# Performance work log

Measured on AMD Instinct MI355X. Metric: run time of the kernel, lower is better.

The kernel has to match this reference:

```python
import jax, jax.numpy as jnp
import numpy as np

DEPTH = 16
PERCENT = 1.2
MAX_P = 5.0
# ps[t] = clip((t+1)*percent, 0, max_percent), as in the torch __init__
PS = np.clip((np.arange(DEPTH) + 1) * PERCENT, 0.0, MAX_P)


def setup_inputs() -> dict:
    key = jax.random.key(0)
    kx, kA = jax.random.split(key, 2)
    B, M, N = 16384, 256, 1024
    A = jax.random.normal(kA, (M, N), dtype=jnp.float32) / np.sqrt(M)
    # L = max eigenvalue of A^T A (as max_eig in the torch code), scaled by 1.001
    gram = np.asarray(A.T @ A)
    L = float(np.linalg.eigvalsh(gram)[-1]) * 1.001
    # init=True initialization: every bias layer weight is A.T / L, threshold = 1/L
    W = jnp.tile((A.T / L)[None, :, :], (DEPTH, 1, 1))  # [depth, N, M]
    threshold = jnp.ones((DEPTH,), dtype=jnp.float32) / L
    x = jax.random.normal(kx, (B, M), dtype=jnp.float32)
    return {"x": x, "A": A, "W": W, "threshold": threshold}


def _shrink(x, t):
    # soft threshold: sign(x) * max(|x| - t, 0)
    return jnp.sign(x) * jnp.maximum(jnp.abs(x) - t, 0.0)


def _shrinkss(x, t, p):
    # support-selection shrink: entries above both the learned threshold and the
    # per-row (100-p) percentile of |x| pass through untouched; the rest are
    # soft-thresholded. Mask and percentile are detached (no_grad in torch).
    n = x.shape[1]
    idx = int(np.ceil((100.0 - p) / 100.0 * n)) - 1  # static per iteration
    abs_x = jnp.abs(x)
    thresh = jax.lax.stop_gradient(jnp.sort(abs_x, axis=1)[:, idx])  # [B]
    mask = jax.lax.stop_gradient(
        ((abs_x >= t) & (abs_x >= thresh[:, None])).astype(x.dtype)
    )
    return mask * x + _shrink((1.0 - mask) * x, t)


def reference(x, A, W, threshold):
    # x: [B, M], A: [M, N], W: [depth, N, M], threshold: [depth]
    B = x.shape[0]
    N = A.shape[1]
    u = jnp.zeros((B, N), dtype=x.dtype)
    for i in range(DEPTH):
        r = x - u @ A.T                      # residual in measurement space [B, M]
        v = u + r @ W[i].T                   # gradient step via learned bias [B, N]
        u = _shrinkss(v, threshold[i], PS[i])
    return u
```

## Files before the change

### kernel.cpp

```cpp
#include <hip/hip_runtime.h>
#include <hip/hip_bf16.h>

#define B_ROWS 16384
#define M_DIM  256
#define N_DIM  1024
#define DEPTH  16

typedef __attribute__((ext_vector_type(8))) short short8;
typedef __attribute__((ext_vector_type(4))) float f32x4;
typedef __attribute__((ext_vector_type(2))) float f32x2;

#define ATP_OFF_B   0
#define WTP_OFF_B   1572864
#define RP_OFF_B    (1572864 + 25165824)
#define TAU_OFF_B   (RP_OFF_B + 25165824)
#define WS_FAST_NEED ((size_t)TAU_OFF_B + 65536)
#define WTP_SLICE   (64 * 8 * 3 * 512)
#define RP_PANEL_US 24576

#define AT_OFF 0
#define WT_OFF (262144)
#define WS_OLD_NEED ((size_t)(262144 + 16 * 262144) * 4)

__device__ __forceinline__ unsigned short bf16r(float f) {
    unsigned u = __float_as_uint(f);
    u += 0x7fffu + ((u >> 16) & 1u);
    return (unsigned short)(u >> 16);
}
__device__ __forceinline__ float bf2f(unsigned short h) {
    return __uint_as_float(((unsigned)h) << 16);
}
__device__ __forceinline__ void split3(float x, unsigned short& h, unsigned short& m,
                                       unsigned short& lo) {
    h = bf16r(x); float r1 = x - bf2f(h);
    m = bf16r(r1); float r2 = r1 - bf2f(m);
    lo = bf16r(r2);
}
__device__ __forceinline__ f32x4 MF(short8 a, short8 b, f32x4 c) {
    return __builtin_amdgcn_mfma_f32_16x16x32_bf16(a, b, c, 0, 0, 0);
}
__device__ __forceinline__ float shrink_one(float v, float t, float thrv) {
    float a = fabsf(v);
    return (a >= thrv) ? v : copysignf(fmaxf(a - t, 0.0f), v);
}

__global__ void prep_a_kernel(const float* __restrict__ A, unsigned short* __restrict__ ATp) {
    int g = blockIdx.x * 256 + threadIdx.x;
    if (g >= 16 * 32 * 64) return;
    int l = g & 63, kc = (g >> 6) & 31, tile = g >> 11;
    int row = tile * 16 + (l & 15);
    int k0 = kc * 32 + ((l >> 4) << 3);
    unsigned short h[8], m[8], lo[8];
#pragma unroll
    for (int j = 0; j < 8; ++j) split3(A[(size_t)row * N_DIM + k0 + j], h[j], m[j], lo[j]);
    size_t base = ((size_t)(tile * 32 + kc) * 3) * 512 + l * 8;
#pragma unroll
    for (int j = 0; j < 8; ++j) {
        ATp[base + j] = h[j];
        ATp[base + 512 + j] = m[j];
        ATp[base + 1024 + j] = lo[j];
    }
}

__global__ void prep_w_kernel(const float* __restrict__ W, unsigned short* __restrict__ WTp) {
    int g = blockIdx.x * 256 + threadIdx.x;
    if (g >= 16 * 64 * 8 * 64) return;
    int l = g & 63, kc = (g >> 6) & 7, tile = (g >> 9) & 63, it = g >> 15;
    int n = tile * 16 + (l & 15);
    int m0 = kc * 32 + ((l >> 4) << 3);
    const float* Wi = W + (size_t)it * N_DIM * M_DIM;
    unsigned short h[8], m[8], lo[8];
#pragma unroll
    for (int j = 0; j < 8; ++j) split3(Wi[(size_t)n * M_DIM + m0 + j], h[j], m[j], lo[j]);
    size_t base = (((size_t)(it * 64 + tile) * 8 + kc) * 3) * 512 + l * 8;
#pragma unroll
    for (int j = 0; j < 8; ++j) {
        WTp[base + j] = h[j];
        WTp[base + 512 + j] = m[j];
        WTp[base + 1024 + j] = lo[j];
    }
}

__global__ void prep_x_kernel(const float* __restrict__ x, unsigned short* __restrict__ RP) {
    int g = blockIdx.x * 256 + threadIdx.x;
    if (g >= 524288) return;
    int l = g & 63, kcp = (g >> 6) & 3, wm = (g >> 8) & 1, c = (g >> 9) & 1, panel = g >> 10;
    int row = panel * 32 + wm * 16 + (l & 15);
    int k0 = c * 128 + kcp * 32 + ((l >> 4) << 3);
    unsigned short h[8], m[8], lo[8];
#pragma unroll
    for (int j = 0; j < 8; ++j) split3(x[(size_t)row * M_DIM + k0 + j], h[j], m[j], lo[j]);
    size_t base = (size_t)panel * RP_PANEL_US + ((((c * 2 + wm) * 4 + kcp) * 3)) * 512 + l * 8;
#pragma unroll
    for (int j = 0; j < 8; ++j) {
        RP[base + j] = h[j];
        RP[base + 512 + j] = m[j];
        RP[base + 1024 + j] = lo[j];
    }
}

#define LSTR2 136
#define BUFUS 13056

__global__ __launch_bounds__(1024)
void g1_kernel(const float* __restrict__ UV, const float* __restrict__ x,
               const unsigned short* __restrict__ ATp,
               const float* __restrict__ thr_all, float* __restrict__ TAU,
               unsigned short* __restrict__ RP, int iter, int kth_prev) {
    __align__(16) __shared__ unsigned short smem[2 * BUFUS];
    __shared__ float tau_s[32];
    const int tid = threadIdx.x;
    const int l = tid & 63, w = tid >> 6;
    const int wm = w >> 3, wn = w & 7;
    const int panel = blockIdx.x;
    const int row0 = panel * 32;
    const int arow = 16 * wm + (l & 15);
    const int akl  = (l >> 4) << 3;
    const float tprev = thr_all[iter - 1];

    {
#pragma unroll 1
        for (int rr = 0; rr < 2; ++rr) {
            const int row = w * 2 + rr;
            const float* vp = UV + (size_t)(row0 + row) * N_DIM;
            unsigned key[16];
#pragma unroll
            for (int j = 0; j < 16; ++j)
                key[j] = __float_as_uint(vp[l + 64 * j]) & 0x7fffffffu;
            unsigned p = 0;
#pragma unroll 1
            for (int b = 30; b >= 0; --b) {
                const unsigned cand = p | (1u << b);
                int cnt = 0;
#pragma unroll
                for (int j = 0; j < 16; ++j) cnt += (key[j] >= cand) ? 1 : 0;
#pragma unroll
                for (int off = 32; off; off >>= 1) cnt += __shfl_xor(cnt, off);
                if (cnt >= kth_prev) p = cand;
            }
            if (l == 0) {
                tau_s[row] = __uint_as_float(p);
                TAU[row0 + row] = __uint_as_float(p);
            }
        }
    }
    __syncthreads();

    f32x4 acc_hi[2], acc_rest[2];
    double acc64[2][4];
#pragma unroll
    for (int t = 0; t < 2; ++t) {
        acc_hi[t] = (f32x4){0, 0, 0, 0};
        acc_rest[t] = (f32x4){0, 0, 0, 0};
#pragma unroll
        for (int e = 0; e < 4; ++e) acc64[t][e] = 0.0;
    }

    f32x2 st[2];
#pragma unroll
    for (int jj = 0; jj < 2; ++jj) {
        const int idx = tid + 1024 * jj;
        const int r = idx >> 6, kq = idx & 63;
        st[jj] = *(const f32x2*)&UV[(size_t)(row0 + r) * N_DIM + kq * 2];
    }
#pragma unroll
    for (int jj = 0; jj < 2; ++jj) {
        const int idx = tid + 1024 * jj;
        const int r = idx >> 6, kq = idx & 63;
        const float thrv = fmaxf(tprev, tau_s[r]);
        const float a0 = shrink_one(st[jj].x, tprev, thrv);
        const float a1 = shrink_one(st[jj].y, tprev, thrv);
        unsigned short h0, m0, lo0, h1, m1, lo1;
        split3(a0, h0, m0, lo0);
        split3(a1, h1, m1, lo1);
        const unsigned off = (unsigned)r * LSTR2 + kq * 2;
        *(unsigned*)&smem[off] = (unsigned)h0 | ((unsigned)h1 << 16);
        *(unsigned*)&smem[4352 + off] = (unsigned)m0 | ((unsigned)m1 << 16);
        *(unsigned*)&smem[8704 + off] = (unsigned)lo0 | ((unsigned)lo1 << 16);
    }
#pragma unroll
    for (int jj = 0; jj < 2; ++jj) {
        const int idx = tid + 1024 * jj;
        const int r = idx >> 6, kq = idx & 63;
        st[jj] = *(const f32x2*)&UV[(size_t)(row0 + r) * N_DIM + 128 + kq * 2];
    }
    __syncthreads();

    for (int c = 0; c < 8; ++c) {
        const unsigned bb = (unsigned)(c & 1) * BUFUS;
        const unsigned nb = (unsigned)((c + 1) & 1) * BUFUS;
        if (c < 7) {
#pragma unroll
            for (int jj = 0; jj < 2; ++jj) {
                const int idx = tid + 1024 * jj;
                const int r = idx >> 6, kq = idx & 63;
                const float thrv = fmaxf(tprev, tau_s[r]);
                const float a0 = shrink_one(st[jj].x, tprev, thrv);
                const float a1 = shrink_one(st[jj].y, tprev, thrv);
                unsigned short h0, m0, lo0, h1, m1, lo1;
                split3(a0, h0, m0, lo0);
                split3(a1, h1, m1, lo1);
                const unsigned off = (unsigned)r * LSTR2 + kq * 2;
                *(unsigned*)&smem[nb + off] = (unsigned)h0 | ((unsigned)h1 << 16);
                *(unsigned*)&smem[nb + 4352 + off] = (unsigned)m0 | ((unsigned)m1 << 16);
                *(unsigned*)&smem[nb + 8704 + off] = (unsigned)lo0 | ((unsigned)lo1 << 16);
            }
        }
        if (c < 6) {
#pragma unroll
            for (int jj = 0; jj < 2; ++jj) {
                const int idx = tid + 1024 * jj;
                const int r = idx >> 6, kq = idx & 63;
                st[jj] = *(const f32x2*)&UV[(size_t)(row0 + r) * N_DIM + (c + 2) * 128 + kq * 2];
            }
        }
#pragma unroll
        for (int kc = 0; kc < 4; ++kc) {
            const unsigned ao = bb + (unsigned)arow * LSTR2 + kc * 32 + akl;
            short8 ah = *(const short8*)&smem[ao];
            short8 am = *(const short8*)&smem[ao + 4352];
            short8 al = *(const short8*)&smem[ao + 8704];
#pragma unroll
            for (int tt = 0; tt < 2; ++tt) {
                const int tile = wn * 2 + tt;
                const unsigned bo = ((unsigned)(tile * 32 + c * 4 + kc) * 3) * 512 + l * 8;
                short8 bh = *(const short8*)&ATp[bo];
                short8 bm = *(const short8*)&ATp[bo + 512];
                short8 bl = *(const short8*)&ATp[bo + 1024];
                acc_hi[tt] = MF(ah, bh, acc_hi[tt]);
                acc_rest[tt] = MF(ah, bm, acc_rest[tt]);
                acc_rest[tt] = MF(am, bh, acc_rest[tt]);
                acc_rest[tt] = MF(am, bm, acc_rest[tt]);
                acc_rest[tt] = MF(ah, bl, acc_rest[tt]);
                acc_rest[tt] = MF(al, bh, acc_rest[tt]);
            }
        }
#pragma unroll
        for (int tt = 0; tt < 2; ++tt) {
#pragma unroll
            for (int e = 0; e < 4; ++e) acc64[tt][e] += (double)acc_hi[tt][e];
            acc_hi[tt] = (f32x4){0, 0, 0, 0};
        }
        __syncthreads();
    }

    {
        const int cimg = wn >> 2, kcp = wn & 3;
        const unsigned fbase = ((((unsigned)(cimg * 2 + wm) * 4 + kcp) * 3)) * 512;
#pragma unroll
        for (int tt = 0; tt < 2; ++tt) {
            const int col = wn * 32 + tt * 16 + (l & 15);
            const int hi2 = (tt * 2 + ((l & 15) >> 3)) & 3;
#pragma unroll
            for (int e = 0; e < 4; ++e) {
                const int rl = ((l >> 4) << 2) + e;
                const int row = row0 + wm * 16 + rl;
                const double tot = acc64[tt][e] + (double)acc_rest[tt][e];
                const float rv = (float)((double)x[(size_t)row * M_DIM + col] - tot);
                unsigned short h, m, lo;
                split3(rv, h, m, lo);
                const unsigned sl = fbase + (unsigned)(hi2 * 16 + rl) * 8 + (l & 7);
                smem[sl] = h;
                smem[sl + 512] = m;
                smem[sl + 1024] = lo;
            }
        }
    }
    __syncthreads();
    {
        const uint4* s4 = (const uint4*)smem;
        uint4* d4 = (uint4*)(RP + (size_t)panel * RP_PANEL_US);
        d4[tid] = s4[tid];
        d4[tid + 1024] = s4[tid + 1024];
        d4[tid + 2048] = s4[tid + 2048];
    }
}

__global__ __launch_bounds__(1024)
void g2_kernel(const unsigned short* __restrict__ RP, const unsigned short* __restrict__ WTpi,
               const float* __restrict__ thr_all, const float* __restrict__ TAU,
               float* UV, int iter) {
    __align__(16) __shared__ unsigned short img[24576];
    const int tid = threadIdx.x;
    const int l = tid & 63, w = tid >> 6;
    const int wm = w >> 3, wn = w & 7;
    const int panel = blockIdx.x >> 2, cg = blockIdx.x & 3;
    const int row0 = panel * 32;

    {
        const uint4* s4 = (const uint4*)(RP + (size_t)panel * RP_PANEL_US);
        uint4* d4 = (uint4*)img;
        d4[tid] = s4[tid];
        d4[tid + 1024] = s4[tid + 1024];
        d4[tid + 2048] = s4[tid + 2048];
    }
    __syncthreads();

    f32x4 hi[2], rest[2], sum[2];
#pragma unroll
    for (int t = 0; t < 2; ++t) {
        hi[t] = (f32x4){0, 0, 0, 0};
        rest[t] = (f32x4){0, 0, 0, 0};
        sum[t] = (f32x4){0, 0, 0, 0};
    }

    for (int kc = 0; kc < 8; ++kc) {
        const unsigned ab = ((((unsigned)(kc >> 2) * 2 + wm) * 4 + (kc & 3)) * 3) * 512 + l * 8;
        short8 ah = *(const short8*)&img[ab];
        short8 am = *(const short8*)&img[ab + 512];
        short8 al = *(const short8*)&img[ab + 1024];
#pragma unroll
        for (int tt = 0; tt < 2; ++tt) {
            const int tile = cg * 16 + wn * 2 + tt;
            const unsigned bo = ((unsigned)(tile * 8 + kc) * 3) * 512 + l * 8;
            short8 bh = *(const short8*)&WTpi[bo];
            short8 bm = *(const short8*)&WTpi[bo + 512];
            short8 bl = *(const short8*)&WTpi[bo + 1024];
            hi[tt] = MF(ah, bh, hi[tt]);
            rest[tt] = MF(ah, bm, rest[tt]);
            rest[tt] = MF(am, bh, rest[tt]);
            rest[tt] = MF(am, bm, rest[tt]);
            rest[tt] = MF(ah, bl, rest[tt]);
            rest[tt] = MF(al, bh, rest[tt]);
        }
        if ((kc & 3) == 3) {
#pragma unroll
            for (int tt = 0; tt < 2; ++tt) {
#pragma unroll
                for (int e = 0; e < 4; ++e) sum[tt][e] += hi[tt][e];
                hi[tt] = (f32x4){0, 0, 0, 0};
            }
        }
    }

    const float tprev = (iter > 0) ? thr_all[iter - 1] : 0.0f;
#pragma unroll
    for (int tt = 0; tt < 2; ++tt) {
        const int col = cg * 256 + wn * 32 + tt * 16 + (l & 15);
#pragma unroll
        for (int e = 0; e < 4; ++e) {
            const int row = row0 + wm * 16 + ((l >> 4) << 2) + e;
            const float tot = sum[tt][e] + rest[tt][e];
            float us = 0.0f;
            if (iter > 0) {
                const float uo = UV[(size_t)row * N_DIM + col];
                const float thrv = fmaxf(tprev, TAU[row]);
                us = shrink_one(uo, tprev, thrv);
            }
            UV[(size_t)row * N_DIM + col] = us + tot;
        }
    }
}

__global__ __launch_bounds__(256)
void s_kernel(float* UV, const float* __restrict__ thr_all, int iter, int kth) {
    __shared__ float v_s[8][1024];
    __shared__ float tau_s[8];
    const int tid = threadIdx.x;
    const int lane = tid & 63;
    const int wave = tid >> 6;
    const int row0 = blockIdx.x * 8;
    const float t = thr_all[iter];
    {
        const float4* Vg4 = (const float4*)(UV + (size_t)row0 * N_DIM);
        float4* vs4 = (float4*)(&v_s[0][0]);
#pragma unroll
        for (int c = 0; c < 8; ++c) vs4[tid + 256 * c] = Vg4[tid + 256 * c];
    }
    __syncthreads();
#pragma unroll 1
    for (int rr = 0; rr < 2; ++rr) {
        const int row = wave + rr * 4;
        unsigned key[16];
#pragma unroll
        for (int j = 0; j < 16; ++j)
            key[j] = __float_as_uint(v_s[row][lane + 64 * j]) & 0x7fffffffu;
        unsigned p = 0;
#pragma unroll 1
        for (int b = 30; b >= 0; --b) {
            const unsigned cand = p | (1u << b);
            int cnt = 0;
#pragma unroll
            for (int j = 0; j < 16; ++j) cnt += (key[j] >= cand) ? 1 : 0;
#pragma unroll
            for (int off = 32; off; off >>= 1) cnt += __shfl_xor(cnt, off);
            if (cnt >= kth) p = cand;
        }
        if (lane == 0) tau_s[row] = __uint_as_float(p);
    }
    __syncthreads();
    {
        const float4* vs4 = (const float4*)&v_s[0][0];
        float4* Uw = (float4*)(UV + (size_t)row0 * N_DIM);
#pragma unroll 1
        for (int c = 0; c < 8; ++c) {
            const int idx = tid + 256 * c;
            const int row = idx >> 8;
            const float thrv = fmaxf(t, tau_s[row]);
            float4 v = vs4[idx];
            float4 o;
            o.x = shrink_one(v.x, t, thrv);
            o.y = shrink_one(v.y, t, thrv);
            o.z = shrink_one(v.z, t, thrv);
            o.w = shrink_one(v.w, t, thrv);
            Uw[idx] = o;
        }
    }
}

#define DFMA4(acc, s, v) do { \
    (acc).x += (double)(s) * (double)(v).x; \
    (acc).y += (double)(s) * (double)(v).y; \
    (acc).z += (double)(s) * (double)(v).z; \
    (acc).w += (double)(s) * (double)(v).w; } while (0)

__global__ void transpose_kernel(const float* __restrict__ in, float* __restrict__ out,
                                 int R, int C) {
    __shared__ float tile[32][33];
    int s = blockIdx.z;
    const float* ip = in + (size_t)s * R * C;
    float* op = out + (size_t)s * R * C;
    int c0 = blockIdx.x * 32, r0 = blockIdx.y * 32;
    int tx = threadIdx.x, ty = threadIdx.y;
#pragma unroll
    for (int k = 0; k < 4; ++k)
        tile[ty + 8 * k][tx] = ip[(size_t)(r0 + ty + 8 * k) * C + (c0 + tx)];
    __syncthreads();
#pragma unroll
    for (int k = 0; k < 4; ++k)
        op[(size_t)(c0 + ty + 8 * k) * R + (r0 + tx)] = tile[tx][ty + 8 * k];
}

__global__ void zero_kernel(float* __restrict__ p, int n) {
    int i = blockIdx.x * blockDim.x + threadIdx.x;
    int stride = gridDim.x * blockDim.x;
    for (; i < n; i += stride) p[i] = 0.0f;
}

template <bool T>
__device__ __forceinline__ float4 loadAT(const float* __restrict__ p, int n, int m4) {
    if constexpr (T) {
        return ((const float4*)p)[n * 64 + m4];
    } else {
        float4 r;
        r.x = p[(size_t)(4 * m4 + 0) * N_DIM + n];
        r.y = p[(size_t)(4 * m4 + 1) * N_DIM + n];
        r.z = p[(size_t)(4 * m4 + 2) * N_DIM + n];
        r.w = p[(size_t)(4 * m4 + 3) * N_DIM + n];
        return r;
    }
}
template <bool T>
__device__ __forceinline__ float4 loadWT(const float* __restrict__ p, int m, int n4) {
    if constexpr (T) {
        return ((const float4*)p)[m * 256 + n4];
    } else {
        float4 r;
        r.x = p[(size_t)(4 * n4 + 0) * M_DIM + m];
        r.y = p[(size_t)(4 * n4 + 1) * M_DIM + m];
        r.z = p[(size_t)(4 * n4 + 2) * M_DIM + m];
        r.w = p[(size_t)(4 * n4 + 3) * M_DIM + m];
        return r;
    }
}

template <bool T>
__global__ __launch_bounds__(256)
void lista_iter_kernel(const float* __restrict__ x, const float* __restrict__ Ap,
                       const float* __restrict__ Wp, const float* __restrict__ thr_all,
                       float* __restrict__ U, int iter, int kth) {
    __shared__ float u_s[8][1024];
    __shared__ float r_s[8][256];
    __shared__ float tau_s[8];
    const int tid = threadIdx.x;
    const int lane = tid & 63;
    const int wave = tid >> 6;
    const int row0 = blockIdx.x * 8;
    const float t = thr_all[iter];
    {
        const float4* Ug4 = (const float4*)(U + (size_t)row0 * N_DIM);
        float4* us4 = (float4*)(&u_s[0][0]);
#pragma unroll
        for (int c = 0; c < 8; ++c) us4[tid + 256 * c] = Ug4[tid + 256 * c];
    }
    __syncthreads();
    {
        double4 acc0 = {0, 0, 0, 0}, acc1 = {0, 0, 0, 0};
        const float4* u0p = (const float4*)&u_s[wave][0];
        const float4* u1p = (const float4*)&u_s[wave + 4][0];
        for (int n4 = 0; n4 < 256; ++n4) {
            float4 u0 = u0p[n4];
            float4 u1 = u1p[n4];
            float4 a0 = loadAT<T>(Ap, 4 * n4 + 0, lane);
            float4 a1 = loadAT<T>(Ap, 4 * n4 + 1, lane);
            float4 a2 = loadAT<T>(Ap, 4 * n4 + 2, lane);
            float4 a3 = loadAT<T>(Ap, 4 * n4 + 3, lane);
            DFMA4(acc0, u0.x, a0); DFMA4(acc0, u0.y, a1); DFMA4(acc0, u0.z, a2); DFMA4(acc0, u0.w, a3);
            DFMA4(acc1, u1.x, a0); DFMA4(acc1, u1.y, a1); DFMA4(acc1, u1.z, a2); DFMA4(acc1, u1.w, a3);
        }
        float4 xv0 = ((const float4*)(x + (size_t)(row0 + wave) * M_DIM))[lane];
        float4 xv1 = ((const float4*)(x + (size_t)(row0 + wave + 4) * M_DIM))[lane];
        float4 rv0, rv1;
        rv0.x = (float)((double)xv0.x - acc0.x);
        rv0.y = (float)((double)xv0.y - acc0.y);
        rv0.z = (float)((double)xv0.z - acc0.z);
        rv0.w = (float)((double)xv0.w - acc0.w);
        rv1.x = (float)((double)xv1.x - acc1.x);
        rv1.y = (float)((double)xv1.y - acc1.y);
        rv1.z = (float)((double)xv1.z - acc1.z);
        rv1.w = (float)((double)xv1.w - acc1.w);
        ((float4*)&r_s[wave][0])[lane] = rv0;
        ((float4*)&r_s[wave + 4][0])[lane] = rv1;
    }
    __syncthreads();
    {
        const float4* r0p = (const float4*)&r_s[wave][0];
        const float4* r1p = (const float4*)&r_s[wave + 4][0];
        float4* u0p = (float4*)&u_s[wave][0];
        float4* u1p = (float4*)&u_s[wave + 4][0];
#pragma unroll 1
        for (int q = 0; q < 4; ++q) {
            const int n4 = lane + 64 * q;
            double4 acc0 = {0, 0, 0, 0}, acc1 = {0, 0, 0, 0};
            for (int m4 = 0; m4 < 64; ++m4) {
                float4 r0 = r0p[m4];
                float4 r1 = r1p[m4];
                float4 w0 = loadWT<T>(Wp, 4 * m4 + 0, n4);
                float4 w1 = loadWT<T>(Wp, 4 * m4 + 1, n4);
                float4 w2 = loadWT<T>(Wp, 4 * m4 + 2, n4);
                float4 w3 = loadWT<T>(Wp, 4 * m4 + 3, n4);
                DFMA4(acc0, r0.x, w0); DFMA4(acc0, r0.y, w1); DFMA4(acc0, r0.z, w2); DFMA4(acc0, r0.w, w3);
                DFMA4(acc1, r1.x, w0); DFMA4(acc1, r1.y, w1); DFMA4(acc1, r1.z, w2); DFMA4(acc1, r1.w, w3);
            }
            float4 uv0 = u0p[n4];
            uv0.x = (float)((double)uv0.x + acc0.x);
            uv0.y = (float)((double)uv0.y + acc0.y);
            uv0.z = (float)((double)uv0.z + acc0.z);
            uv0.w = (float)((double)uv0.w + acc0.w);
            u0p[n4] = uv0;
            float4 uv1 = u1p[n4];
            uv1.x = (float)((double)uv1.x + acc1.x);
            uv1.y = (float)((double)uv1.y + acc1.y);
            uv1.z = (float)((double)uv1.z + acc1.z);
            uv1.w = (float)((double)uv1.w + acc1.w);
            u1p[n4] = uv1;
        }
    }
    __syncthreads();
    {
#pragma unroll 1
        for (int rr = 0; rr < 2; ++rr) {
            const int row = wave + rr * 4;
            unsigned key[16];
#pragma unroll
            for (int j = 0; j < 16; ++j)
                key[j] = __float_as_uint(u_s[row][lane + 64 * j]) & 0x7fffffffu;
            unsigned p = 0;
#pragma unroll 1
            for (int b = 30; b >= 0; --b) {
                const unsigned cand = p | (1u << b);
                int cnt = 0;
#pragma unroll
                for (int j = 0; j < 16; ++j) cnt += (key[j] >= cand) ? 1 : 0;
#pragma unroll
                for (int off = 32; off; off >>= 1) cnt += __shfl_xor(cnt, off);
                if (cnt >= kth) p = cand;
            }
            if (lane == 0) tau_s[row] = __uint_as_float(p);
        }
    }
    __syncthreads();
    {
        const float4* us4 = (const float4*)&u_s[0][0];
        float4* Uw = (float4*)(U + (size_t)row0 * N_DIM);
#pragma unroll 1
        for (int c = 0; c < 8; ++c) {
            const int idx = tid + 256 * c;
            const int row = idx >> 8;
            const float thrv = fmaxf(t, tau_s[row]);
            float4 v = us4[idx];
            float4 o;
            o.x = shrink_one(v.x, t, thrv);
            o.y = shrink_one(v.y, t, thrv);
            o.z = shrink_one(v.z, t, thrv);
            o.w = shrink_one(v.w, t, thrv);
            Uw[idx] = o;
        }
    }
}

extern "C" void kernel_launch(void* const* d_in, const int* in_sizes, int n_in,
                              void* d_out, int out_size, void* d_ws, size_t ws_size,
                              hipStream_t stream) {
    const float* x   = (const float*)d_in[0];
    const float* A   = (const float*)d_in[1];
    const float* W   = (const float*)d_in[2];
    const float* thr = (const float*)d_in[3];

    float* UV = (float*)d_out;

    static const int ktab[DEPTH] = {13, 25, 37, 50, 52, 52, 52, 52,
                                    52, 52, 52, 52, 52, 52, 52, 52};

    if (ws_size >= WS_FAST_NEED) {
        unsigned short* ATp = (unsigned short*)((char*)d_ws + ATP_OFF_B);
        unsigned short* WTp = (unsigned short*)((char*)d_ws + WTP_OFF_B);
        unsigned short* RP  = (unsigned short*)((char*)d_ws + RP_OFF_B);
        float* TAU = (float*)((char*)d_ws + TAU_OFF_B);

        prep_a_kernel<<<128, 256, 0, stream>>>(A, ATp);
        prep_w_kernel<<<2048, 256, 0, stream>>>(W, WTp);
        prep_x_kernel<<<2048, 256, 0, stream>>>(x, RP);

        g2_kernel<<<2048, 1024, 0, stream>>>(RP, WTp, thr, TAU, UV, 0);

        for (int it = 1; it < DEPTH; ++it) {
            g1_kernel<<<512, 1024, 0, stream>>>(UV, x, ATp, thr, TAU, RP, it,
                                                ktab[it - 1]);
            g2_kernel<<<2048, 1024, 0, stream>>>(RP, WTp + (size_t)it * WTP_SLICE,
                                                 thr, TAU, UV, it);
        }
        s_kernel<<<B_ROWS / 8, 256, 0, stream>>>(UV, thr, DEPTH - 1, ktab[DEPTH - 1]);
    } else if (ws_size >= WS_OLD_NEED) {
        float* ws = (float*)d_ws;
        float* AT = ws + AT_OFF;
        float* WT = ws + WT_OFF;
        zero_kernel<<<1024, 256, 0, stream>>>(UV, B_ROWS * N_DIM);
        dim3 tb(32, 8);
        transpose_kernel<<<dim3(N_DIM / 32, M_DIM / 32, 1), tb, 0, stream>>>(A, AT, M_DIM, N_DIM);
        transpose_kernel<<<dim3(M_DIM / 32, N_DIM / 32, DEPTH), tb, 0, stream>>>(W, WT, N_DIM, M_DIM);
        for (int it = 0; it < DEPTH; ++it)
            lista_iter_kernel<true><<<B_ROWS / 8, 256, 0, stream>>>(
                x, AT, WT + (size_t)it * M_DIM * N_DIM, thr, UV, it, ktab[it]);
    } else {
        zero_kernel<<<1024, 256, 0, stream>>>(UV, B_ROWS * N_DIM);
        for (int it = 0; it < DEPTH; ++it)
            lista_iter_kernel<false><<<B_ROWS / 8, 256, 0, stream>>>(
                x, A, W + (size_t)it * N_DIM * M_DIM, thr, UV, it, ktab[it]);
    }
}
```

Measured before the change: 3.182 ms.

## Split shrink into a separate in-place kernel before g1 and g2

Adds a separate kernel that, per row, finds the percentile threshold by a bitwise radix search using ballot/popcount counting and writes the shrunk values back into UV in place. g1 and g2 then read UV as already-shrunk values, so they no longer compute thresholds, recompute shrink per element or use the TAU buffer. This removes the redundant shrink work inside the GEMM kernels and the in-g1 threshold search that stalled all waves before a block barrier. The cost is an extra kernel launch and an extra full read and write pass over UV each iteration.

```diff
diff --git a/kernel.cpp b/kernel.cpp
--- a/kernel.cpp
+++ b/kernel.cpp
@@ -13,8 +13,7 @@
 #define ATP_OFF_B   0
 #define WTP_OFF_B   1572864
 #define RP_OFF_B    (1572864 + 25165824)
-#define TAU_OFF_B   (RP_OFF_B + 25165824)
-#define WS_FAST_NEED ((size_t)TAU_OFF_B + 65536)
+#define WS_FAST_NEED ((size_t)RP_OFF_B + 25165824)
 #define WTP_SLICE   (64 * 8 * 3 * 512)
 #define RP_PANEL_US 24576
 
@@ -99,16 +98,44 @@
     }
 }
 
+__global__ __launch_bounds__(1024)
+void spp_kernel(float* __restrict__ UV, const float* __restrict__ thr_all,
+                int iter, int kth) {
+    const int l = threadIdx.x & 63;
+    const int w = threadIdx.x >> 6;
+    const int row = blockIdx.x * 16 + w;
+    const float t = thr_all[iter];
+    float* vp = UV + (size_t)row * N_DIM;
+    float v[16]; unsigned key[16];
+#pragma unroll
+    for (int j = 0; j < 16; ++j) {
+        v[j] = vp[l + 64 * j];
+        key[j] = __float_as_uint(v[j]) & 0x7fffffffu;
+    }
+    unsigned p = 0;
+#pragma unroll 1
+    for (int b = 30; b >= 0; --b) {
+        const unsigned cand = p | (1u << b);
+        int cnt = 0;
+#pragma unroll
+        for (int j = 0; j < 16; ++j)
+            cnt += __popcll(__ballot(key[j] >= cand));
+        if (cnt >= kth) p = cand;
+    }
+    const float thrv = fmaxf(t, __uint_as_float(p));
+#pragma unroll
+    for (int j = 0; j < 16; ++j)
+        vp[l + 64 * j] = shrink_one(v[j], t, thrv);
+}
+
 #define LSTR2 136
 #define BUFUS 13056
 
 __global__ __launch_bounds__(1024)
 void g1_kernel(const float* __restrict__ UV, const float* __restrict__ x,
                const unsigned short* __restrict__ ATp,
-               const float* __restrict__ thr_all, float* __restrict__ TAU,
-               unsigned short* __restrict__ RP, int iter, int kth_prev) {
+               unsigned short* __restrict__ RP) {
     __align__(16) __shared__ unsigned short smem[2 * BUFUS];
-    __shared__ float tau_s[32];
     const int tid = threadIdx.x;
     const int l = tid & 63, w = tid >> 6;
     const int wm = w >> 3, wn = w & 7;
@@ -116,35 +143,6 @@
     const int row0 = panel * 32;
     const int arow = 16 * wm + (l & 15);
     const int akl  = (l >> 4) << 3;
-    const float tprev = thr_all[iter - 1];
-
-    {
-#pragma unroll 1
-        for (int rr = 0; rr < 2; ++rr) {
-            const int row = w * 2 + rr;
-            const float* vp = UV + (size_t)(row0 + row) * N_DIM;
-            unsigned key[16];
-#pragma unroll
-            for (int j = 0; j < 16; ++j)
-                key[j] = __float_as_uint(vp[l + 64 * j]) & 0x7fffffffu;
-            unsigned p = 0;
-#pragma unroll 1
-            for (int b = 30; b >= 0; --b) {
-                const unsigned cand = p | (1u << b);
-                int cnt = 0;
-#pragma unroll
-                for (int j = 0; j < 16; ++j) cnt += (key[j] >= cand) ? 1 : 0;
-#pragma unroll
-                for (int off = 32; off; off >>= 1) cnt += __shfl_xor(cnt, off);
-                if (cnt >= kth_prev) p = cand;
-            }
-            if (l == 0) {
-                tau_s[row] = __uint_as_float(p);
-                TAU[row0 + row] = __uint_as_float(p);
-            }
-        }
-    }
-    __syncthreads();
 
     f32x4 acc_hi[2], acc_rest[2];
     double acc64[2][4];
@@ -167,12 +165,9 @@
     for (int jj = 0; jj < 2; ++jj) {
         const int idx = tid + 1024 * jj;
         const int r = idx >> 6, kq = idx & 63;
-        const float thrv = fmaxf(tprev, tau_s[r]);
-        const float a0 = shrink_one(st[jj].x, tprev, thrv);
-        const float a1 = shrink_one(st[jj].y, tprev, thrv);
         unsigned short h0, m0, lo0, h1, m1, lo1;
-        split3(a0, h0, m0, lo0);
-        split3(a1, h1, m1, lo1);
+        split3(st[jj].x, h0, m0, lo0);
+        split3(st[jj].y, h1, m1, lo1);
         const unsigned off = (unsigned)r * LSTR2 + kq * 2;
         *(unsigned*)&smem[off] = (unsigned)h0 | ((unsigned)h1 << 16);
         *(unsigned*)&smem[4352 + off] = (unsigned)m0 | ((unsigned)m1 << 16);
@@ -194,12 +189,9 @@
             for (int jj = 0; jj < 2; ++jj) {
                 const int idx = tid + 1024 * jj;
                 const int r = idx >> 6, kq = idx & 63;
-                const float thrv = fmaxf(tprev, tau_s[r]);
-                const float a0 = shrink_one(st[jj].x, tprev, thrv);
-                const float a1 = shrink_one(st[jj].y, tprev, thrv);
                 unsigned short h0, m0, lo0, h1, m1, lo1;
-                split3(a0, h0, m0, lo0);
-                split3(a1, h1, m1, lo1);
+                split3(st[jj].x, h0, m0, lo0);
+                split3(st[jj].y, h1, m1, lo1);
                 const unsigned off = (unsigned)r * LSTR2 + kq * 2;
                 *(unsigned*)&smem[nb + off] = (unsigned)h0 | ((unsigned)h1 << 16);
                 *(unsigned*)&smem[nb + 4352 + off] = (unsigned)m0 | ((unsigned)m1 << 16);
@@ -278,7 +270,6 @@
 
 __global__ __launch_bounds__(1024)
 void g2_kernel(const unsigned short* __restrict__ RP, const unsigned short* __restrict__ WTpi,
-               const float* __restrict__ thr_all, const float* __restrict__ TAU,
                float* UV, int iter) {
     __align__(16) __shared__ unsigned short img[24576];
     const int tid = threadIdx.x;
@@ -333,7 +324,6 @@
         }
     }
 
-    const float tprev = (iter > 0) ? thr_all[iter - 1] : 0.0f;
 #pragma unroll
     for (int tt = 0; tt < 2; ++tt) {
         const int col = cg * 256 + wn * 32 + tt * 16 + (l & 15);
@@ -341,12 +331,7 @@
         for (int e = 0; e < 4; ++e) {
             const int row = row0 + wm * 16 + ((l >> 4) << 2) + e;
             const float tot = sum[tt][e] + rest[tt][e];
-            float us = 0.0f;
-            if (iter > 0) {
-                const float uo = UV[(size_t)row * N_DIM + col];
-                const float thrv = fmaxf(tprev, TAU[row]);
-                us = shrink_one(uo, tprev, thrv);
-            }
+            const float us = (iter > 0) ? UV[(size_t)row * N_DIM + col] : 0.0f;
             UV[(size_t)row * N_DIM + col] = us + tot;
         }
     }
@@ -606,19 +591,17 @@
         unsigned short* ATp = (unsigned short*)((char*)d_ws + ATP_OFF_B);
         unsigned short* WTp = (unsigned short*)((char*)d_ws + WTP_OFF_B);
         unsigned short* RP  = (unsigned short*)((char*)d_ws + RP_OFF_B);
-        float* TAU = (float*)((char*)d_ws + TAU_OFF_B);
 
         prep_a_kernel<<<128, 256, 0, stream>>>(A, ATp);
         prep_w_kernel<<<2048, 256, 0, stream>>>(W, WTp);
         prep_x_kernel<<<2048, 256, 0, stream>>>(x, RP);
 
-        g2_kernel<<<2048, 1024, 0, stream>>>(RP, WTp, thr, TAU, UV, 0);
+        g2_kernel<<<2048, 1024, 0, stream>>>(RP, WTp, UV, 0);
 
         for (int it = 1; it < DEPTH; ++it) {
-            g1_kernel<<<512, 1024, 0, stream>>>(UV, x, ATp, thr, TAU, RP, it,
-                                                ktab[it - 1]);
-            g2_kernel<<<2048, 1024, 0, stream>>>(RP, WTp + (size_t)it * WTP_SLICE,
-                                                 thr, TAU, UV, it);
+            spp_kernel<<<B_ROWS / 16, 1024, 0, stream>>>(UV, thr, it - 1, ktab[it - 1]);
+            g1_kernel<<<512, 1024, 0, stream>>>(UV, x, ATp, RP);
+            g2_kernel<<<2048, 1024, 0, stream>>>(RP, WTp + (size_t)it * WTP_SLICE, UV, it);
         }
         s_kernel<<<B_ROWS / 8, 256, 0, stream>>>(UV, thr, DEPTH - 1, ktab[DEPTH - 1]);
     } else if (ws_size >= WS_OLD_NEED) {
```

Result: no change. 3.127 ms (-1.7%).
